# Kernel optimization log

Measured on AMD Instinct MI355X. Metric: run time of the kernel, lower is better.

Reference implementation:

```python
import jax, jax.numpy as jnp
import numpy as np

BQ, BP, L, CIN, H1, H2, COUT = 32, 256, 16, 8192, 256, 32, 8192


def _conv_block(x, w1, b1, w2, b2, w3, b3):
    # x: (B, L, H1) -> Conv1d stack over token dim with residual, as in self.convs
    h = jnp.transpose(x, (0, 2, 1))  # (B, H1, L)
    for w, b in ((w1, b1), (w2, b2), (w3, b3)):
        h = jax.lax.conv_general_dilated(h, w, (1,), [(2, 2)],
                                         dimension_numbers=('NCH', 'OIH', 'NCH'))
        h = jax.nn.relu(h + b[None, :, None])
    return jnp.transpose(h, (0, 2, 1)) + x


def setup_inputs() -> dict:
    key = jax.random.key(0)
    ks = jax.random.split(key, 16)
    query_x = (jax.random.uniform(ks[0], (BQ, L, CIN)) < 0.01).astype(jnp.float32)
    poi_x = (jax.random.uniform(ks[1], (BP, L, CIN)) < 0.01).astype(jnp.float32)
    query_loc = jax.random.uniform(ks[2], (BQ, 2)) * 100.0
    poi_loc = jax.random.uniform(ks[3], (BP, 2)) * 100.0
    enc_w = jax.random.normal(ks[4], (H1, CIN)) * 0.02
    conv_w1 = jax.random.normal(ks[5], (H1, H1, 5)) * 0.02
    conv_w2 = jax.random.normal(ks[6], (H1, H1, 5)) * 0.02
    conv_w3 = jax.random.normal(ks[7], (H1, H1, 5)) * 0.02
    conv_b1 = jnp.zeros((H1,), jnp.float32)
    conv_b2 = jnp.zeros((H1,), jnp.float32)
    conv_b3 = jnp.zeros((H1,), jnp.float32)
    dec_w1 = jax.random.normal(ks[8], (H2, 2 * H1)) * 0.05
    dec_b1 = jnp.zeros((H2,), jnp.float32)
    dec_w2 = jax.random.normal(ks[9], (H2, H2)) * 0.1
    dec_b2 = jnp.zeros((H2,), jnp.float32)
    # torch init fills this with 0; use small randn so the path is non-trivial
    dec_w3 = jax.random.normal(ks[10], (COUT, H2)) * 0.01
    a = jnp.asarray(1.0, jnp.float32)
    b = jnp.asarray(0.0, jnp.float32)
    c = jnp.asarray(1.0, jnp.float32)
    d = jnp.asarray(0.0, jnp.float32)
    return dict(query_x=query_x, query_loc=query_loc, poi_x=poi_x, poi_loc=poi_loc,
                enc_w=enc_w, conv_w1=conv_w1, conv_b1=conv_b1, conv_w2=conv_w2,
                conv_b2=conv_b2, conv_w3=conv_w3, conv_b3=conv_b3,
                dec_w1=dec_w1, dec_b1=dec_b1, dec_w2=dec_w2, dec_b2=dec_b2,
                dec_w3=dec_w3, a=a, b=b, c=c, d=d)


def reference(query_x, query_loc, poi_x, poi_loc, enc_w, conv_w1, conv_b1,
              conv_w2, conv_b2, conv_w3, conv_b3, dec_w1, dec_b1, dec_w2,
              dec_b2, dec_w3, a, b, c, d):
    # --- encode ---
    q_h = _conv_block(query_x @ enc_w.T, conv_w1, conv_b1, conv_w2, conv_b2, conv_w3, conv_b3)
    p_h = _conv_block(poi_x @ enc_w.T, conv_w1, conv_b1, conv_w2, conv_b2, conv_w3, conv_b3)
    q_emb = q_h.mean(axis=1)  # (Bq, H1)
    p_emb = p_h.mean(axis=1)  # (Bp, H1)
    # --- bloom masks ---
    q_bloom = jnp.minimum(query_x.sum(axis=1), 1.0)  # (Bq, 8192)
    p_bloom = jnp.minimum(poi_x.sum(axis=1), 1.0)    # (Bp, 8192)
    interaction = q_bloom[:, None, :] * p_bloom[None, :, :]  # (Bq, Bp, 8192)
    q_bits = q_bloom.sum(axis=-1, keepdims=True)             # (Bq, 1)
    # --- pairwise MLP decode ---
    bq, bp = q_emb.shape[0], p_emb.shape[0]
    all_embed = jnp.concatenate([
        jnp.broadcast_to(q_emb[:, None, :], (bq, bp, q_emb.shape[-1])),
        jnp.broadcast_to(p_emb[None, :, :], (bq, bp, p_emb.shape[-1])),
    ], axis=-1)  # (Bq, Bp, 2*H1)
    h = jax.nn.relu(all_embed)
    h = jax.nn.relu(h @ dec_w1.T + dec_b1)
    h = jax.nn.relu(h @ dec_w2.T + dec_b2)
    w = h @ dec_w3.T  # (Bq, Bp, 8192)
    weights = jnp.where(w >= 0, w, w * 0.125) + 1.0  # LeakyReLU(1/8) + 1
    desc_sim = (interaction * weights).sum(axis=-1) / q_bits  # (Bq, Bp)
    # --- geo-distance fusion ---
    dist = jnp.sqrt(((query_loc[:, None, :] - poi_loc[None, :, :]) ** 2).sum(axis=-1))
    mean = desc_sim.mean(axis=-1, keepdims=True)
    std = jnp.std(desc_sim, axis=-1, keepdims=True, ddof=1)  # torch.std is unbiased
    desc_sim = (desc_sim - mean) / (std + 1e-6)
    dist_sim = -jnp.log(dist + 1.0)
    return (c - jax.nn.sigmoid(a * desc_sim + b)) * (dist_sim - d)
```

## Files before the change

### kernel.cpp

```cpp
#include <hip/hip_runtime.h>

#define NB 288
#define NBQ 32
#define NBP 256
#define LTOK 16
#define CIN 8192
#define H1 256
#define H2 32
#define MASKW 256
#define XROW 264

typedef __attribute__((ext_vector_type(8))) short short8;
typedef __attribute__((ext_vector_type(4))) float f32x4;

__device__ __forceinline__ unsigned short f2bf(float f) {
    unsigned u = __float_as_uint(f);
    u += 0x7fffu + ((u >> 16) & 1u);
    return (unsigned short)(u >> 16);
}

__global__ __launch_bounds__(256) void k_prep(const float* __restrict__ encw,
                                              const float* __restrict__ w1,
                                              const float* __restrict__ w2,
                                              const float* __restrict__ w3c,
                                              const float* __restrict__ dw3,
                                              unsigned* __restrict__ wtp,
                                              unsigned short* __restrict__ wtb,
                                              unsigned* __restrict__ w3p,
                                              unsigned* __restrict__ masks,
                                              float* __restrict__ esum,
                                              float* __restrict__ Cmat) {
    int g = blockIdx.x, tid = threadIdx.x;
    if (g < 2048) {
        __shared__ float tile[32][33];
        int k0 = (g >> 3) * 32, h0 = (g & 7) * 32;
        int tx = tid & 31, ty = tid >> 5;
#pragma unroll
        for (int i = 0; i < 32; i += 8)
            tile[ty + i][tx] = encw[(h0 + ty + i) * CIN + k0 + tx];
        __syncthreads();
        int kl = tid >> 3, pw = tid & 7;
#pragma unroll
        for (int u = 0; u < 2; ++u) {
            int p = pw + u * 8;
            unsigned lo = f2bf(tile[2 * p][kl]);
            unsigned hi = f2bf(tile[2 * p + 1][kl]);
            wtp[(size_t)(k0 + kl) * 128 + (h0 >> 1) + p] = (hi << 16) | lo;
        }
    } else if (g < 5888) {
        int bx = g - 2048;
        int l = bx / 1280;
        int r = bx - l * 1280;
        int o = r / 5;
        int d = r - o * 5;
        const float* w = (l == 0) ? w1 : (l == 1) ? w2 : w3c;
        wtb[(size_t)l * 327680 + (size_t)o * 1280 + d * 256 + tid] =
            f2bf(w[(size_t)o * 1280 + tid * 5 + d]);
    } else if (g < 6400) {
        int idx = (g - 5888) * 256 + tid;
        int k = idx >> 4, pw = idx & 15;
        unsigned lo = f2bf(dw3[k * 32 + 2 * pw]);
        unsigned hi = f2bf(dw3[k * 32 + 2 * pw + 1]);
        w3p[idx] = (hi << 16) | lo;
    } else {
        int b = g - 6400;
        masks[b * MASKW + tid] = 0u;
        esum[b * 256 + tid] = 0.f;
        if (tid < 32) Cmat[b * 32 + tid] = 0.f;
        if (b == 0 && tid < 128) wtp[(size_t)8192 * 128 + tid] = 0u;
    }
}

__global__ __launch_bounds__(256) void k_scanG(const float* __restrict__ qx,
                                               const float* __restrict__ px,
                                               const unsigned* __restrict__ wtp,
                                               unsigned* __restrict__ masks,
                                               float* __restrict__ esum,
                                               unsigned* __restrict__ xbufu) {
    int row = blockIdx.x;
    int b = row >> 4;
    const float* x = (b < NBQ) ? (qx + (size_t)row * CIN)
                               : (px + (size_t)(row - NBQ * LTOK) * CIN);
    __shared__ int idxs[200];
    __shared__ int cnt;
    __shared__ float sL[2][128], sH[2][128];
    int tid = threadIdx.x;
    if (tid == 0) cnt = 0;
    __syncthreads();
    const float4* x4 = (const float4*)x;
    float4 r[8];
#pragma unroll
    for (int j = 0; j < 8; ++j) r[j] = x4[j * 256 + tid];
#pragma unroll
    for (int j = 0; j < 8; ++j) {
        unsigned ox = __float_as_uint(r[j].x) | __float_as_uint(r[j].y) |
                      __float_as_uint(r[j].z) | __float_as_uint(r[j].w);
        if (ox) {
            int base = (j * 256 + tid) * 4;
            float vv[4] = {r[j].x, r[j].y, r[j].z, r[j].w};
#pragma unroll
            for (int c = 0; c < 4; ++c) {
                if (vv[c] != 0.f) {
                    int k = base + c;
                    int p = atomicAdd(&cnt, 1);
                    if (p < 192) idxs[p] = k;
                    atomicOr(&masks[b * MASKW + (k >> 5)], 1u << (k & 31));
                }
            }
        }
    }
    __syncthreads();
    int n = min(cnt, 192);
    for (int i = n + tid; i < 200; i += 256) idxs[i] = 8192;
    __syncthreads();
    int pair = tid & 127, half = tid >> 7;
    float aL = 0.f, aH = 0.f;
    for (int j0 = 0; j0 < n; j0 += 8) {
        int4 ia = *(const int4*)(idxs + j0 + half * 4);
        int id[4] = {ia.x, ia.y, ia.z, ia.w};
#pragma unroll
        for (int u = 0; u < 4; ++u) {
            unsigned v = wtp[(size_t)id[u] * 128 + pair];
            aL += __uint_as_float(v << 16);
            aH += __uint_as_float(v & 0xffff0000u);
        }
    }
    sL[half][pair] = aL; sH[half][pair] = aH;
    __syncthreads();
    if (tid < 128) {
        float L = sL[0][tid] + sL[1][tid];
        float H = sH[0][tid] + sH[1][tid];
        atomicAdd(&esum[b * 256 + 2 * tid],     L);
        atomicAdd(&esum[b * 256 + 2 * tid + 1], H);
        unsigned bl = f2bf(L), bh = f2bf(H);
        xbufu[(size_t)row * 128 + tid] = (bh << 16) | bl;
    }
}

__global__ __launch_bounds__(256) void k_cgemm(const unsigned short* __restrict__ actIn,
                                               unsigned short* __restrict__ actOut,
                                               const unsigned short* __restrict__ wl,
                                               const float* __restrict__ bias) {
    __shared__ unsigned short Als[2 * 20 * XROW];
    __shared__ unsigned short Bls[32 * XROW];
    int tid = threadIdx.x;
    int m0 = blockIdx.x * 32, n0 = blockIdx.y * 32;

    int* Ai = (int*)Als;
#pragma unroll
    for (int i = tid; i < 20 * XROW; i += 256) Ai[i] = 0;
    __syncthreads();

    int row = tid >> 3, part = tid & 7;
    {
        const short8* src = (const short8*)(actIn + (size_t)(m0 + row) * 256 + part * 32);
        unsigned short* dst = Als + ((row >> 4) * 20 + (row & 15) + 2) * XROW + part * 32;
#pragma unroll
        for (int j = 0; j < 4; ++j) *(short8*)(dst + j * 8) = src[j];
    }
    const unsigned short* bsrc = wl + (size_t)(n0 + row) * 1280 + part * 32;
    short8 rb[4];
#pragma unroll
    for (int j = 0; j < 4; ++j) rb[j] = *(const short8*)(bsrc + j * 8);

    int lane = tid & 63, wave = tid >> 6;
    int lane15 = lane & 15, quad = lane >> 4;
    int wm = wave & 1, wn = wave >> 1;
    unsigned short* bdst = Bls + row * XROW + part * 32;

    f32x4 acc = (f32x4){0.f, 0.f, 0.f, 0.f};
#pragma unroll 1
    for (int d = 0; d < 5; ++d) {
#pragma unroll
        for (int j = 0; j < 4; ++j) *(short8*)(bdst + j * 8) = rb[j];
        __syncthreads();
        if (d < 4) {
            const unsigned short* s2 = bsrc + (d + 1) * 256;
#pragma unroll
            for (int j = 0; j < 4; ++j) rb[j] = *(const short8*)(s2 + j * 8);
        }
        const unsigned short* ap = Als + (wm * 20 + lane15 + d) * XROW + quad * 8;
        const unsigned short* bp = Bls + (wn * 16 + lane15) * XROW + quad * 8;
#pragma unroll
        for (int kk = 0; kk < 8; ++kk) {
            short8 av = *(const short8*)(ap + kk * 32);
            short8 bv = *(const short8*)(bp + kk * 32);
            acc = __builtin_amdgcn_mfma_f32_16x16x32_bf16(av, bv, acc, 0, 0, 0);
        }
        __syncthreads();
    }

    int o = n0 + wn * 16 + lane15;
    float bv = bias[o];
    int rbase = m0 + wm * 16 + quad * 4;
#pragma unroll
    for (int r = 0; r < 4; ++r)
        actOut[(size_t)(rbase + r) * 256 + o] = f2bf(fmaxf(acc[r] + bv, 0.f));
}

__global__ __launch_bounds__(256) void k_cgemm3(const unsigned short* __restrict__ actIn,
                                                const unsigned short* __restrict__ wl,
                                                const float* __restrict__ bias,
                                                const float* __restrict__ esum,
                                                const float* __restrict__ dw1,
                                                float* __restrict__ Cmat) {
    __shared__ unsigned short Als[2 * 20 * XROW];
    __shared__ unsigned short Bls[32 * XROW];
    __shared__ float els[2][32];
    int tid = threadIdx.x;
    int m0 = blockIdx.x * 32, n0 = blockIdx.y * 32;

    int* Ai = (int*)Als;
#pragma unroll
    for (int i = tid; i < 20 * XROW; i += 256) Ai[i] = 0;
    __syncthreads();

    int row = tid >> 3, part = tid & 7;
    {
        const short8* src = (const short8*)(actIn + (size_t)(m0 + row) * 256 + part * 32);
        unsigned short* dst = Als + ((row >> 4) * 20 + (row & 15) + 2) * XROW + part * 32;
#pragma unroll
        for (int j = 0; j < 4; ++j) *(short8*)(dst + j * 8) = src[j];
    }
    const unsigned short* bsrc = wl + (size_t)(n0 + row) * 1280 + part * 32;
    short8 rb[4];
#pragma unroll
    for (int j = 0; j < 4; ++j) rb[j] = *(const short8*)(bsrc + j * 8);

    int lane = tid & 63, wave = tid >> 6;
    int lane15 = lane & 15, quad = lane >> 4;
    int wm = wave & 1, wn = wave >> 1;
    unsigned short* bdst = Bls + row * XROW + part * 32;

    f32x4 acc = (f32x4){0.f, 0.f, 0.f, 0.f};
#pragma unroll 1
    for (int d = 0; d < 5; ++d) {
#pragma unroll
        for (int j = 0; j < 4; ++j) *(short8*)(bdst + j * 8) = rb[j];
        __syncthreads();
        if (d < 4) {
            const unsigned short* s2 = bsrc + (d + 1) * 256;
#pragma unroll
            for (int j = 0; j < 4; ++j) rb[j] = *(const short8*)(s2 + j * 8);
        }
        const unsigned short* ap = Als + (wm * 20 + lane15 + d) * XROW + quad * 8;
        const unsigned short* bp = Bls + (wn * 16 + lane15) * XROW + quad * 8;
#pragma unroll
        for (int kk = 0; kk < 8; ++kk) {
            short8 av = *(const short8*)(ap + kk * 32);
            short8 bv = *(const short8*)(bp + kk * 32);
            acc = __builtin_amdgcn_mfma_f32_16x16x32_bf16(av, bv, acc, 0, 0, 0);
        }
        __syncthreads();
    }

    int o_l = wn * 16 + lane15;
    int o = n0 + o_l;
    float bv = bias[o];
    float sf = 0.f;
#pragma unroll
    for (int r = 0; r < 4; ++r) sf += fmaxf(acc[r] + bv, 0.f);
    sf += __shfl_xor(sf, 16, 64);
    sf += __shfl_xor(sf, 32, 64);
    if (quad == 0) {
        int bb = 2 * blockIdx.x + wm;
        els[wm][o_l] = fmaxf((sf + esum[bb * 256 + o]) * (1.f / 16.f), 0.f);
    }
    __syncthreads();
    if (tid < 64) {
        int b2 = tid >> 5, op = tid & 31;
        int bb = 2 * blockIdx.x + b2;
        const float* wr = dw1 + (size_t)op * 512 + (bb < NBQ ? 0 : 256) + n0;
        float s = 0.f;
#pragma unroll
        for (int j = 0; j < 32; ++j) s = fmaf(wr[j], els[b2][j], s);
        atomicAdd(&Cmat[bb * 32 + op], s);
    }
}

__global__ __launch_bounds__(256) void k_pair(const float* __restrict__ Cmat,
                                              const float* __restrict__ b1,
                                              const float* __restrict__ w2,
                                              const float* __restrict__ b2,
                                              const unsigned* __restrict__ w3p,
                                              const unsigned* __restrict__ masks,
                                              float* __restrict__ desc) {
    int p = blockIdx.x, q = blockIdx.y;
    __shared__ float h1[32];
    __shared__ __align__(16) float h2s[32];
    __shared__ int idxs[3072];
    __shared__ int cnt;
    __shared__ float wsum[4], wq[4];
    int tid = threadIdx.x;
    if (tid == 0) cnt = 0;
    __syncthreads();
    unsigned mq = masks[q * MASKW + tid];
    unsigned m = mq & masks[(NBQ + p) * MASKW + tid];
    int nb = __popc(m);
    if (nb) {
        int pos = atomicAdd(&cnt, nb);
        while (m) {
            int bit = __ffs(m) - 1;
            m &= m - 1;
            idxs[pos++] = tid * 32 + bit;
        }
    }
    if (tid < 32)
        h1[tid] = fmaxf(Cmat[q * 32 + tid] + Cmat[(NBQ + p) * 32 + tid] + b1[tid], 0.f);
    __syncthreads();
    if (tid < 32) {
        float s = b2[tid];
#pragma unroll
        for (int j = 0; j < 32; ++j) s = fmaf(w2[tid * 32 + j], h1[j], s);
        h2s[tid] = fmaxf(s, 0.f);
    }
    __syncthreads();
    int n = cnt;
    int rowi = tid >> 2, part = tid & 3;
    float h2v[8];
#pragma unroll
    for (int j = 0; j < 8; ++j) h2v[j] = h2s[part * 8 + j];
    float local = 0.f;
    for (int base = 0; base < n; base += 64) {
        int r = base + rowi;
        bool act = r < n;
        float dot = 0.f;
        if (act) {
            uint4 wv = *(const uint4*)(w3p + (size_t)idxs[r] * 16 + part * 4);
            unsigned wu[4] = {wv.x, wv.y, wv.z, wv.w};
#pragma unroll
            for (int u = 0; u < 4; ++u) {
                dot += __uint_as_float(wu[u] << 16) * h2v[2 * u];
                dot += __uint_as_float(wu[u] & 0xffff0000u) * h2v[2 * u + 1];
            }
        }
        dot += __shfl_xor(dot, 1);
        dot += __shfl_xor(dot, 2);
        if (act && part == 0)
            local += 1.f + (dot >= 0.f ? dot : dot * 0.125f);
    }
    float qcf = (float)__popc(mq);
#pragma unroll
    for (int st = 1; st < 64; st <<= 1) {
        local += __shfl_xor(local, st);
        qcf   += __shfl_xor(qcf, st);
    }
    if ((tid & 63) == 0) { wsum[tid >> 6] = local; wq[tid >> 6] = qcf; }
    __syncthreads();
    if (tid == 0) {
        float t  = wsum[0] + wsum[1] + wsum[2] + wsum[3];
        float qb = wq[0] + wq[1] + wq[2] + wq[3];
        desc[q * 256 + p] = t / qb;
    }
}

__global__ __launch_bounds__(256) void k_final(const float* __restrict__ desc,
                                               const float* __restrict__ qloc,
                                               const float* __restrict__ ploc,
                                               const float* __restrict__ sa,
                                               const float* __restrict__ sb,
                                               const float* __restrict__ sc,
                                               const float* __restrict__ sd,
                                               float* __restrict__ out) {
    __shared__ float red[256];
    int q = blockIdx.x, tid = threadIdx.x;
    float v = desc[q * 256 + tid];
    red[tid] = v; __syncthreads();
    for (int st = 128; st > 0; st >>= 1) {
        if (tid < st) red[tid] += red[tid + st];
        __syncthreads();
    }
    float mean = red[0] * (1.f / 256.f);
    __syncthreads();
    float dv = v - mean;
    red[tid] = dv * dv; __syncthreads();
    for (int st = 128; st > 0; st >>= 1) {
        if (tid < st) red[tid] += red[tid + st];
        __syncthreads();
    }
    float var = red[0] * (1.f / 255.f);
    float norm = dv / (sqrtf(var) + 1e-6f);
    float dx = qloc[q * 2]     - ploc[tid * 2];
    float dy = qloc[q * 2 + 1] - ploc[tid * 2 + 1];
    float dist = sqrtf(dx * dx + dy * dy);
    float z = sa[0] * norm + sb[0];
    float sig = 1.f / (1.f + expf(-z));
    out[q * 256 + tid] = (sc[0] - sig) * (-logf(dist + 1.f) - sd[0]);
}

extern "C" void kernel_launch(void* const* d_in, const int* in_sizes, int n_in,
                              void* d_out, int out_size, void* d_ws, size_t ws_size,
                              hipStream_t stream) {
    const float* qx   = (const float*)d_in[0];
    const float* qloc = (const float*)d_in[1];
    const float* px   = (const float*)d_in[2];
    const float* ploc = (const float*)d_in[3];
    const float* encw = (const float*)d_in[4];
    const float* cw1  = (const float*)d_in[5];
    const float* cb1  = (const float*)d_in[6];
    const float* cw2  = (const float*)d_in[7];
    const float* cb2  = (const float*)d_in[8];
    const float* cw3  = (const float*)d_in[9];
    const float* cb3  = (const float*)d_in[10];
    const float* dw1  = (const float*)d_in[11];
    const float* db1  = (const float*)d_in[12];
    const float* dw2  = (const float*)d_in[13];
    const float* db2  = (const float*)d_in[14];
    const float* dw3  = (const float*)d_in[15];
    const float* sa   = (const float*)d_in[16];
    const float* sb   = (const float*)d_in[17];
    const float* sc   = (const float*)d_in[18];
    const float* sd   = (const float*)d_in[19];

    char* w = (char*)d_ws;
    unsigned*       wtp   = (unsigned*)w;       w += (size_t)8193 * 128 * 4;
    unsigned short* xbuf  = (unsigned short*)w; w += (size_t)NB * LTOK * H1 * 2;
    unsigned short* act1  = (unsigned short*)w; w += (size_t)NB * LTOK * H1 * 2;
    unsigned short* act2  = (unsigned short*)w; w += (size_t)NB * LTOK * H1 * 2;
    unsigned short* wtb   = (unsigned short*)w; w += (size_t)3 * 256 * 1280 * 2;
    unsigned*       w3p   = (unsigned*)w;       w += (size_t)CIN * 16 * 4;
    float*          esum  = (float*)w;          w += (size_t)NB * H1 * 4;
    float*          Cmat  = (float*)w;          w += (size_t)NB * H2 * 4;
    unsigned*       masks = (unsigned*)w;       w += (size_t)NB * MASKW * 4;
    float*          desc  = (float*)w;          w += (size_t)NBQ * NBP * 4;

    k_prep<<<6688, 256, 0, stream>>>(encw, cw1, cw2, cw3, dw3,
                                     wtp, wtb, w3p, masks, esum, Cmat);
    k_scanG<<<NB * LTOK, 256, 0, stream>>>(qx, px, wtp, masks, esum, (unsigned*)xbuf);
    dim3 cgrid(NB * LTOK / 32, 8);
    k_cgemm<<<cgrid, 256, 0, stream>>>(xbuf, act1, wtb,          cb1);
    k_cgemm<<<cgrid, 256, 0, stream>>>(act1, act2, wtb + 327680, cb2);
    k_cgemm3<<<cgrid, 256, 0, stream>>>(act2, wtb + 2 * 327680, cb3, esum, dw1, Cmat);
    k_pair<<<dim3(NBP, NBQ), 256, 0, stream>>>(Cmat, db1, dw2, db2, w3p, masks, desc);
    k_final<<<NBQ, 256, 0, stream>>>(desc, qloc, ploc, sa, sb, sc, sd, (float*)d_out);
}
```

Measured before the change: 333.8 us.

## Load conv weights straight into registers, drop esum atomics, prefetch pair rows

The conv GEMM kernels stop staging weight tiles through shared memory. Each wave now loads its B fragments directly from global memory into registers, which removes the per-tap barriers, and only the zero-padding rows of the activation tile are cleared. The residual token sum in cgemm3 is recomputed from the bf16 xbuf instead of fp32 atomics into an esum buffer, which drops those atomics and their zeroing but adds bf16 rounding to the residual. The pair kernel software-prefetches the next w3p row to hide gather latency.

```diff
diff --git a/kernel.cpp b/kernel.cpp
--- a/kernel.cpp
+++ b/kernel.cpp
@@ -18,6 +18,9 @@
     u += 0x7fffu + ((u >> 16) & 1u);
     return (unsigned short)(u >> 16);
 }
+__device__ __forceinline__ float bf2f(unsigned short u) {
+    return __uint_as_float(((unsigned)u) << 16);
+}
 
 __global__ __launch_bounds__(256) void k_prep(const float* __restrict__ encw,
                                               const float* __restrict__ w1,
@@ -28,7 +31,6 @@
                                               unsigned short* __restrict__ wtb,
                                               unsigned* __restrict__ w3p,
                                               unsigned* __restrict__ masks,
-                                              float* __restrict__ esum,
                                               float* __restrict__ Cmat) {
     int g = blockIdx.x, tid = threadIdx.x;
     if (g < 2048) {
@@ -65,7 +67,6 @@
     } else {
         int b = g - 6400;
         masks[b * MASKW + tid] = 0u;
-        esum[b * 256 + tid] = 0.f;
         if (tid < 32) Cmat[b * 32 + tid] = 0.f;
         if (b == 0 && tid < 128) wtp[(size_t)8192 * 128 + tid] = 0u;
     }
@@ -75,7 +76,6 @@
                                                const float* __restrict__ px,
                                                const unsigned* __restrict__ wtp,
                                                unsigned* __restrict__ masks,
-                                               float* __restrict__ esum,
                                                unsigned* __restrict__ xbufu) {
     int row = blockIdx.x;
     int b = row >> 4;
@@ -130,8 +130,6 @@
     if (tid < 128) {
         float L = sL[0][tid] + sL[1][tid];
         float H = sH[0][tid] + sH[1][tid];
-        atomicAdd(&esum[b * 256 + 2 * tid],     L);
-        atomicAdd(&esum[b * 256 + 2 * tid + 1], H);
         unsigned bl = f2bf(L), bh = f2bf(H);
         xbufu[(size_t)row * 128 + tid] = (bh << 16) | bl;
     }
@@ -142,14 +140,8 @@
                                                const unsigned short* __restrict__ wl,
                                                const float* __restrict__ bias) {
     __shared__ unsigned short Als[2 * 20 * XROW];
-    __shared__ unsigned short Bls[32 * XROW];
     int tid = threadIdx.x;
     int m0 = blockIdx.x * 32, n0 = blockIdx.y * 32;
-
-    int* Ai = (int*)Als;
-#pragma unroll
-    for (int i = tid; i < 20 * XROW; i += 256) Ai[i] = 0;
-    __syncthreads();
 
     int row = tid >> 3, part = tid & 7;
     {
@@ -158,62 +150,54 @@
 #pragma unroll
         for (int j = 0; j < 4; ++j) *(short8*)(dst + j * 8) = src[j];
     }
-    const unsigned short* bsrc = wl + (size_t)(n0 + row) * 1280 + part * 32;
-    short8 rb[4];
-#pragma unroll
-    for (int j = 0; j < 4; ++j) rb[j] = *(const short8*)(bsrc + j * 8);
+    if (tid < 132) {
+        int* Az = (int*)Als;
+#pragma unroll
+        for (int pr = 0; pr < 8; ++pr) {
+            const int rr[8] = {0, 1, 18, 19, 20, 21, 38, 39};
+            Az[rr[pr] * 132 + tid] = 0;
+        }
+    }
 
     int lane = tid & 63, wave = tid >> 6;
     int lane15 = lane & 15, quad = lane >> 4;
     int wm = wave & 1, wn = wave >> 1;
-    unsigned short* bdst = Bls + row * XROW + part * 32;
+    const unsigned short* bsrc = wl + (size_t)(n0 + wn * 16 + lane15) * 1280 + quad * 8;
+    __syncthreads();
 
     f32x4 acc = (f32x4){0.f, 0.f, 0.f, 0.f};
-#pragma unroll 1
+#pragma unroll
     for (int d = 0; d < 5; ++d) {
-#pragma unroll
-        for (int j = 0; j < 4; ++j) *(short8*)(bdst + j * 8) = rb[j];
-        __syncthreads();
-        if (d < 4) {
-            const unsigned short* s2 = bsrc + (d + 1) * 256;
-#pragma unroll
-            for (int j = 0; j < 4; ++j) rb[j] = *(const short8*)(s2 + j * 8);
-        }
+        short8 bv[8];
+#pragma unroll
+        for (int kk = 0; kk < 8; ++kk)
+            bv[kk] = *(const short8*)(bsrc + d * 256 + kk * 32);
         const unsigned short* ap = Als + (wm * 20 + lane15 + d) * XROW + quad * 8;
-        const unsigned short* bp = Bls + (wn * 16 + lane15) * XROW + quad * 8;
 #pragma unroll
         for (int kk = 0; kk < 8; ++kk) {
             short8 av = *(const short8*)(ap + kk * 32);
-            short8 bv = *(const short8*)(bp + kk * 32);
-            acc = __builtin_amdgcn_mfma_f32_16x16x32_bf16(av, bv, acc, 0, 0, 0);
-        }
-        __syncthreads();
+            acc = __builtin_amdgcn_mfma_f32_16x16x32_bf16(av, bv[kk], acc, 0, 0, 0);
+        }
     }
 
     int o = n0 + wn * 16 + lane15;
-    float bv = bias[o];
+    float bvv = bias[o];
     int rbase = m0 + wm * 16 + quad * 4;
 #pragma unroll
     for (int r = 0; r < 4; ++r)
-        actOut[(size_t)(rbase + r) * 256 + o] = f2bf(fmaxf(acc[r] + bv, 0.f));
+        actOut[(size_t)(rbase + r) * 256 + o] = f2bf(fmaxf(acc[r] + bvv, 0.f));
 }
 
 __global__ __launch_bounds__(256) void k_cgemm3(const unsigned short* __restrict__ actIn,
                                                 const unsigned short* __restrict__ wl,
                                                 const float* __restrict__ bias,
-                                                const float* __restrict__ esum,
+                                                const unsigned short* __restrict__ xbuf,
                                                 const float* __restrict__ dw1,
                                                 float* __restrict__ Cmat) {
     __shared__ unsigned short Als[2 * 20 * XROW];
-    __shared__ unsigned short Bls[32 * XROW];
     __shared__ float els[2][32];
     int tid = threadIdx.x;
     int m0 = blockIdx.x * 32, n0 = blockIdx.y * 32;
-
-    int* Ai = (int*)Als;
-#pragma unroll
-    for (int i = tid; i < 20 * XROW; i += 256) Ai[i] = 0;
-    __syncthreads();
 
     int row = tid >> 3, part = tid & 7;
     {
@@ -222,49 +206,51 @@
 #pragma unroll
         for (int j = 0; j < 4; ++j) *(short8*)(dst + j * 8) = src[j];
     }
-    const unsigned short* bsrc = wl + (size_t)(n0 + row) * 1280 + part * 32;
-    short8 rb[4];
-#pragma unroll
-    for (int j = 0; j < 4; ++j) rb[j] = *(const short8*)(bsrc + j * 8);
+    if (tid < 132) {
+        int* Az = (int*)Als;
+#pragma unroll
+        for (int pr = 0; pr < 8; ++pr) {
+            const int rr[8] = {0, 1, 18, 19, 20, 21, 38, 39};
+            Az[rr[pr] * 132 + tid] = 0;
+        }
+    }
 
     int lane = tid & 63, wave = tid >> 6;
     int lane15 = lane & 15, quad = lane >> 4;
     int wm = wave & 1, wn = wave >> 1;
-    unsigned short* bdst = Bls + row * XROW + part * 32;
+    const unsigned short* bsrc = wl + (size_t)(n0 + wn * 16 + lane15) * 1280 + quad * 8;
+    __syncthreads();
 
     f32x4 acc = (f32x4){0.f, 0.f, 0.f, 0.f};
-#pragma unroll 1
+#pragma unroll
     for (int d = 0; d < 5; ++d) {
-#pragma unroll
-        for (int j = 0; j < 4; ++j) *(short8*)(bdst + j * 8) = rb[j];
-        __syncthreads();
-        if (d < 4) {
-            const unsigned short* s2 = bsrc + (d + 1) * 256;
-#pragma unroll
-            for (int j = 0; j < 4; ++j) rb[j] = *(const short8*)(s2 + j * 8);
-        }
+        short8 bv[8];
+#pragma unroll
+        for (int kk = 0; kk < 8; ++kk)
+            bv[kk] = *(const short8*)(bsrc + d * 256 + kk * 32);
         const unsigned short* ap = Als + (wm * 20 + lane15 + d) * XROW + quad * 8;
-        const unsigned short* bp = Bls + (wn * 16 + lane15) * XROW + quad * 8;
 #pragma unroll
         for (int kk = 0; kk < 8; ++kk) {
             short8 av = *(const short8*)(ap + kk * 32);
-            short8 bv = *(const short8*)(bp + kk * 32);
-            acc = __builtin_amdgcn_mfma_f32_16x16x32_bf16(av, bv, acc, 0, 0, 0);
-        }
-        __syncthreads();
+            acc = __builtin_amdgcn_mfma_f32_16x16x32_bf16(av, bv[kk], acc, 0, 0, 0);
+        }
     }
 
     int o_l = wn * 16 + lane15;
     int o = n0 + o_l;
-    float bv = bias[o];
+    float bvv = bias[o];
     float sf = 0.f;
 #pragma unroll
-    for (int r = 0; r < 4; ++r) sf += fmaxf(acc[r] + bv, 0.f);
+    for (int r = 0; r < 4; ++r) sf += fmaxf(acc[r] + bvv, 0.f);
     sf += __shfl_xor(sf, 16, 64);
     sf += __shfl_xor(sf, 32, 64);
     if (quad == 0) {
         int bb = 2 * blockIdx.x + wm;
-        els[wm][o_l] = fmaxf((sf + esum[bb * 256 + o]) * (1.f / 16.f), 0.f);
+        float rs = 0.f;
+#pragma unroll
+        for (int t = 0; t < 16; ++t)
+            rs += bf2f(xbuf[((size_t)bb * 16 + t) * 256 + o]);
+        els[wm][o_l] = fmaxf((sf + rs) * (1.f / 16.f), 0.f);
     }
     __syncthreads();
     if (tid < 64) {
@@ -321,23 +307,27 @@
 #pragma unroll
     for (int j = 0; j < 8; ++j) h2v[j] = h2s[part * 8 + j];
     float local = 0.f;
-    for (int base = 0; base < n; base += 64) {
-        int r = base + rowi;
-        bool act = r < n;
-        float dot = 0.f;
-        if (act) {
-            uint4 wv = *(const uint4*)(w3p + (size_t)idxs[r] * 16 + part * 4);
+    if (n > 0) {
+        bool act = rowi < n;
+        uint4 wv = *(const uint4*)(w3p + (size_t)idxs[act ? rowi : 0] * 16 + part * 4);
+        for (int base = 0; base < n; base += 64) {
+            int rn = base + 64 + rowi;
+            bool actn = rn < n;
+            uint4 nv = *(const uint4*)(w3p + (size_t)idxs[actn ? rn : 0] * 16 + part * 4);
+            float dot = 0.f;
             unsigned wu[4] = {wv.x, wv.y, wv.z, wv.w};
 #pragma unroll
             for (int u = 0; u < 4; ++u) {
                 dot += __uint_as_float(wu[u] << 16) * h2v[2 * u];
                 dot += __uint_as_float(wu[u] & 0xffff0000u) * h2v[2 * u + 1];
             }
-        }
-        dot += __shfl_xor(dot, 1);
-        dot += __shfl_xor(dot, 2);
-        if (act && part == 0)
-            local += 1.f + (dot >= 0.f ? dot : dot * 0.125f);
+            dot += __shfl_xor(dot, 1);
+            dot += __shfl_xor(dot, 2);
+            if (act && part == 0)
+                local += 1.f + (dot >= 0.f ? dot : dot * 0.125f);
+            wv = nv;
+            act = actn;
+        }
     }
     float qcf = (float)__popc(mq);
 #pragma unroll
@@ -419,18 +409,17 @@
     unsigned short* act2  = (unsigned short*)w; w += (size_t)NB * LTOK * H1 * 2;
     unsigned short* wtb   = (unsigned short*)w; w += (size_t)3 * 256 * 1280 * 2;
     unsigned*       w3p   = (unsigned*)w;       w += (size_t)CIN * 16 * 4;
-    float*          esum  = (float*)w;          w += (size_t)NB * H1 * 4;
     float*          Cmat  = (float*)w;          w += (size_t)NB * H2 * 4;
     unsigned*       masks = (unsigned*)w;       w += (size_t)NB * MASKW * 4;
     float*          desc  = (float*)w;          w += (size_t)NBQ * NBP * 4;
 
     k_prep<<<6688, 256, 0, stream>>>(encw, cw1, cw2, cw3, dw3,
-                                     wtp, wtb, w3p, masks, esum, Cmat);
-    k_scanG<<<NB * LTOK, 256, 0, stream>>>(qx, px, wtp, masks, esum, (unsigned*)xbuf);
+                                     wtp, wtb, w3p, masks, Cmat);
+    k_scanG<<<NB * LTOK, 256, 0, stream>>>(qx, px, wtp, masks, (unsigned*)xbuf);
     dim3 cgrid(NB * LTOK / 32, 8);
     k_cgemm<<<cgrid, 256, 0, stream>>>(xbuf, act1, wtb,          cb1);
     k_cgemm<<<cgrid, 256, 0, stream>>>(act1, act2, wtb + 327680, cb2);
-    k_cgemm3<<<cgrid, 256, 0, stream>>>(act2, wtb + 2 * 327680, cb3, esum, dw1, Cmat);
+    k_cgemm3<<<cgrid, 256, 0, stream>>>(act2, wtb + 2 * 327680, cb3, xbuf, dw1, Cmat);
     k_pair<<<dim3(NBP, NBQ), 256, 0, stream>>>(Cmat, db1, dw2, db2, w3p, masks, desc);
     k_final<<<NBQ, 256, 0, stream>>>(desc, qloc, ploc, sa, sb, sc, sd, (float*)d_out);
 }
```

Result: slower. 362.8 us (+8.7%).
